# Kernel optimization log

Measured on AMD Instinct MI355X. Metric: run time of the kernel, lower is better.

## Reference

```python
import jax, jax.numpy as jnp
from jax import lax
import numpy as np

B, V, H, K, E = 256, 30000, 512, 200, 300
SH_ALPHA = 20.0
REC_W = 0.7
N_ITERS = 100       # fixed iteration budget (original caps at 5000; convergence check freezes updates)
STOP_THR = 0.005
BN_EPS = 1e-3


def setup_inputs() -> dict:
    key = jax.random.key(0)
    ks = jax.random.split(key, 8)
    n = lambda k, shape, scale: (jax.random.normal(k, shape, jnp.float32) * scale)
    return {
        "bows": jax.random.uniform(ks[0], (B, V), jnp.float32),
        "W1": n(ks[1], (H, V), 0.01),
        "b1": jnp.zeros((H,), jnp.float32),
        "W2": n(ks[2], (K, H), 0.05),
        "b2": jnp.zeros((K,), jnp.float32),
        "gamma": jnp.ones((K,), jnp.float32),
        "beta": jnp.zeros((K,), jnp.float32),
        "word_emb": n(ks[3], (V, E), 0.1),
        "topic_emb": n(ks[4], (K, E), 0.1),
    }


def _l2norm(x):
    return x / jnp.maximum(jnp.linalg.norm(x, axis=1, keepdims=True), 1e-12)


def _sinkhorn(cost, kernel, a, b):
    # a: [K,B], b: [V,B], kernel: [K,V]
    u0 = jnp.ones_like(a) / a.shape[0]
    v0 = jnp.ones_like(b)

    def body(carry, i):
        u, v, err = carry
        active = err > STOP_THR
        # u = a / (kernel @ (b / (u^T kernel)^T))
        u1 = a / (kernel @ (b / (u.T @ kernel).T))

        def check(_):
            v1 = b / (kernel.T @ u1)
            u2 = a / (kernel @ v1)
            bb = v1 * (kernel.T @ u2)
            e = jnp.max(jnp.sum(jnp.abs(bb - b), axis=0))
            return u2, v1, e

        # original does the v-refresh + err check when steps % 20 == 1 (steps = i+1)
        u1, v1, e1 = lax.cond(i % 20 == 0, check, lambda _: (u1, v, err), None)
        u = jnp.where(active, u1, u)
        v = jnp.where(active, v1, v)
        err = jnp.where(active, e1, err)
        return (u, v, err), None

    (u, v, _), _ = lax.scan(jax.checkpoint(body), (u0, v0, jnp.asarray(1.0, a.dtype)),
                            jnp.arange(N_ITERS))
    # per-document sinkhorn cost: sum_k u * ((kernel*cost) @ v)
    return jnp.sum(u * ((kernel * cost) @ v), axis=0)  # [B]


def reference(bows, W1, b1, W2, b2, gamma, beta, word_emb, topic_emb):
    # encoder (training-mode BN with batch stats; dropout disabled for determinism)
    h = jax.nn.relu(bows @ W1.T + b1)                      # [B,H]
    z = h @ W2.T + b2                                      # [B,K]
    mu = jnp.mean(z, axis=0)
    var = jnp.var(z, axis=0)                               # biased, as torch BN uses
    zn = gamma * (z - mu) / jnp.sqrt(var + BN_EPS) + beta
    doc_topic = jax.nn.softmax(zn, axis=1)                 # [B,K]

    topic_word = _l2norm(topic_emb) @ _l2norm(word_emb).T  # [K,V]
    cost = 1.0 - topic_word
    kernel = jnp.exp(-cost * SH_ALPHA)

    doc_word = jax.nn.softmax(bows, axis=1)                # [B,V]
    sinkhorn_loss = _sinkhorn(cost, kernel, doc_topic.T, doc_word.T).mean()

    rec_log_probs = jax.nn.log_softmax(doc_topic @ topic_word, axis=1)  # [B,V]
    reconstruction_loss = -(rec_log_probs * bows).sum(axis=1).mean()
    return REC_W * reconstruction_loss, sinkhorn_loss
```

## Files before the change

kernel.cpp:

```cpp
#include <hip/hip_runtime.h>
#include <math.h>

#define CDIV(a,b) (((a)+(b)-1)/(b))

typedef unsigned short u16;
typedef unsigned long long u64;
typedef __attribute__((ext_vector_type(8))) short bf16x8;
typedef __attribute__((ext_vector_type(4))) float f32x4;

constexpr int Bn = 256;
constexpr int Vn = 30000;
constexpr int Hn = 512;
constexpr int Kn = 200;
constexpr int En = 300;
constexpr int E3 = 320;
constexpr int Kp = 224;
constexpr int Vc = 224;
constexpr int NCH = 136;
constexpr int CPX = NCH / 8;
constexpr int Vpad = NCH * Vc;
constexpr int SW1 = 32;
constexpr float ALPHA  = 20.0f;
constexpr float RECW   = 0.7f;
constexpr float THRC   = 0.005f;
constexpr float EPS_BN = 1e-3f;
constexpr int   NIT    = 100;

__device__ __forceinline__ float bf2f(u16 h) {
  union { unsigned u; float f; } c; c.u = (unsigned)h << 16; return c.f;
}
__device__ __forceinline__ u16 f2bf(float f) {
  union { float f; unsigned u; } c; c.f = f;
  return (u16)((c.u + 0x7fffu + ((c.u >> 16) & 1u)) >> 16);
}
__device__ __forceinline__ bf16x8 load8bf(const float* p) {
  float4 a = *(const float4*)p, b = *(const float4*)(p + 4);
  bf16x8 r;
  r[0] = (short)f2bf(a.x); r[1] = (short)f2bf(a.y);
  r[2] = (short)f2bf(a.z); r[3] = (short)f2bf(a.w);
  r[4] = (short)f2bf(b.x); r[5] = (short)f2bf(b.y);
  r[6] = (short)f2bf(b.z); r[7] = (short)f2bf(b.w);
  return r;
}

template<int MODE>
__global__ __launch_bounds__(256, 3)
void fusedAB(const u16* __restrict__ kernT, const u16* __restrict__ kernA,
             const u16* __restrict__ ub, const u16* __restrict__ bmb,
             u16* __restrict__ wout, const u16* __restrict__ win,
             u16* __restrict__ tpart, float* __restrict__ errp,
             const int* __restrict__ frozen)
{
  if (MODE != 3 && frozen[0]) return;
  const int bid = blockIdx.x;
  const int xcd = bid & 7, wid = bid >> 3;
  const int c = xcd * CPX + (wid >> 2), g = wid & 3;
  const int v0 = c * Vc, b0 = g * 64;
  const int tid = threadIdx.x;
  const int wv = tid >> 6, l = tid & 63, l15 = l & 15, lg = l >> 4;
  const int rloc = wv * 16 + l15;
  const int bcol = b0 + rloc;
  __shared__ u16 wlds[64 * Vc];
  char* wbase = (char*)wlds;
  const int sw = (rloc & 3) << 4;

  if (MODE != 3) {
    bf16x8 uf[7];
    {
      const u16* up = ub + (size_t)bcol * Kp + lg * 8;
#pragma unroll
      for (int ks = 0; ks < 7; ++ks) uf[ks] = *(const bf16x8*)(up + ks * 32);
    }
    float e = 0.f;
    for (int vt = 0; vt < Vc / 16; ++vt) {
      const u16* ktp = kernT + (size_t)(v0 + vt * 16 + l15) * Kp + lg * 8;
      f32x4 acc = {0.f, 0.f, 0.f, 0.f};
#pragma unroll
      for (int ks = 0; ks < 7; ++ks) {
        bf16x8 kf = *(const bf16x8*)(ktp + ks * 32);
        acc = __builtin_amdgcn_mfma_f32_16x16x32_bf16(kf, uf[ks], acc, 0, 0, 0);
      }
      const int vbase = v0 + vt * 16 + lg * 4;
      const size_t po = (size_t)bcol * Vpad + vbase;
      u64 bq = *(const u64*)(bmb + po);
      if (MODE == 2) {
        u64 wq = *(const u64*)(win + po);
#pragma unroll
        for (int r = 0; r < 4; ++r) {
          float bm = bf2f((u16)(bq >> (16 * r)));
          float wv_ = bf2f((u16)(wq >> (16 * r)));
          e += fabsf(wv_ * acc[r] - bm);
        }
      } else {
        u64 wq = 0;
#pragma unroll
        for (int r = 0; r < 4; ++r) {
          float bm = bf2f((u16)(bq >> (16 * r)));
          float w = (vbase + r < Vn) ? bm / acc[r] : 0.f;
          wq |= (u64)f2bf(w) << (16 * r);
        }
        *(u64*)(wbase + rloc * (Vc * 2) + ((vt * 32 + lg * 8) ^ sw)) = wq;
        if (MODE == 1) *(u64*)(wout + po) = wq;
      }
    }
    if (MODE == 2) {
      e += __shfl_xor(e, 16, 64);
      e += __shfl_xor(e, 32, 64);
      if (l < 16) errp[c * Bn + bcol] = e;
      return;
    }
    __syncthreads();
  }

  f32x4 accB[13];
#pragma unroll
  for (int mt = 0; mt < 13; ++mt) accB[mt] = (f32x4){0.f, 0.f, 0.f, 0.f};
  for (int vs = 0; vs < Vc / 32; ++vs) {
    bf16x8 wf;
    if (MODE == 3) wf = *(const bf16x8*)(win + (size_t)bcol * Vpad + v0 + vs * 32 + lg * 8);
    else wf = *(const bf16x8*)(wbase + rloc * (Vc * 2) + (((vs * 32 + lg * 8) * 2) ^ sw));
    const u16* kap = kernA + (size_t)l15 * Vpad + v0 + vs * 32 + lg * 8;
#pragma unroll
    for (int mt = 0; mt < 13; ++mt) {
      bf16x8 af = *(const bf16x8*)(kap + (size_t)mt * 16 * Vpad);
      accB[mt] = __builtin_amdgcn_mfma_f32_16x16x32_bf16(af, wf, accB[mt], 0, 0, 0);
    }
  }
#pragma unroll
  for (int mt = 0; mt < 13; ++mt) {
#pragma unroll
    for (int r = 0; r < 4; ++r) {
      int k = mt * 16 + lg * 4 + r;
      if (k < Kn) tpart[((size_t)c * Kn + k) * Bn + bcol] = f2bf(accB[mt][r]);
    }
  }
}

__global__ __launch_bounds__(256, 2)
void reconMF(const u16* __restrict__ costT, const u16* __restrict__ dtb,
             u16* __restrict__ rbuf)
{
  const int c = blockIdx.x, g = blockIdx.y;
  const int v0 = c * Vc, b0 = g * 64;
  const int tid = threadIdx.x;
  const int wv = tid >> 6, l = tid & 63, l15 = l & 15, lg = l >> 4;
  const int bcol = b0 + wv * 16 + l15;
  bf16x8 uf[7];
  {
    const u16* up = dtb + (size_t)bcol * Kp + lg * 8;
#pragma unroll
    for (int ks = 0; ks < 7; ++ks) uf[ks] = *(const bf16x8*)(up + ks * 32);
  }
  for (int vt = 0; vt < Vc / 16; ++vt) {
    const u16* ktp = costT + (size_t)(v0 + vt * 16 + l15) * Kp + lg * 8;
    f32x4 acc = {0.f, 0.f, 0.f, 0.f};
#pragma unroll
    for (int ks = 0; ks < 7; ++ks) {
      bf16x8 kf = *(const bf16x8*)(ktp + ks * 32);
      acc = __builtin_amdgcn_mfma_f32_16x16x32_bf16(kf, uf[ks], acc, 0, 0, 0);
    }
    const int vbase = v0 + vt * 16 + lg * 4;
    u64 q = 0;
#pragma unroll
    for (int r = 0; r < 4; ++r) q |= (u64)f2bf(1.f - acc[r]) << (16 * r);
    *(u64*)(rbuf + (size_t)bcol * Vpad + vbase) = q;
  }
}

__global__ __launch_bounds__(256)
void gemmTW(const u16* __restrict__ nth, const u16* __restrict__ ntl,
            const u16* __restrict__ nwh, const u16* __restrict__ nwl,
            u16* __restrict__ kern_bf, u16* __restrict__ kc_bf,
            u16* __restrict__ cost_bf)
{
  const int n0 = blockIdx.x * 64;
  const int tid = threadIdx.x;
  const int wv = tid >> 6, l = tid & 63, l15 = l & 15, lg = l >> 4;
  const int n = n0 + wv * 16 + l15;
  const bool nok = n < Vn;
  f32x4 acc[14];
#pragma unroll
  for (int mt = 0; mt < 14; ++mt) acc[mt] = (f32x4){0.f, 0.f, 0.f, 0.f};
  for (int kc = 0; kc < E3; kc += 32) {
    bf16x8 bh = {0,0,0,0,0,0,0,0}, bl = {0,0,0,0,0,0,0,0};
    if (nok) {
      const size_t o = (size_t)n * E3 + kc + lg * 8;
      bh = *(const bf16x8*)(nwh + o);
      bl = *(const bf16x8*)(nwl + o);
    }
#pragma unroll
    for (int mt = 0; mt < 14; ++mt) {
      const size_t ao = (size_t)(mt * 16 + l15) * E3 + kc + lg * 8;
      bf16x8 ah = *(const bf16x8*)(nth + ao);
      bf16x8 al = *(const bf16x8*)(ntl + ao);
      acc[mt] = __builtin_amdgcn_mfma_f32_16x16x32_bf16(ah, bh, acc[mt], 0, 0, 0);
      acc[mt] = __builtin_amdgcn_mfma_f32_16x16x32_bf16(ah, bl, acc[mt], 0, 0, 0);
      acc[mt] = __builtin_amdgcn_mfma_f32_16x16x32_bf16(al, bh, acc[mt], 0, 0, 0);
    }
  }
#pragma unroll
  for (int mt = 0; mt < 14; ++mt) {
#pragma unroll
    for (int r = 0; r < 4; ++r) {
      int k = mt * 16 + lg * 4 + r;
      float cf = 1.f - acc[mt][r];
      float kf = expf(-ALPHA * cf);
      size_t o = (size_t)k * Vpad + n;
      kern_bf[o] = f2bf(kf);
      kc_bf[o]   = f2bf(kf * cf);
      cost_bf[o] = f2bf(cf);
    }
  }
}

__global__ __launch_bounds__(256)
void gemmW1(const float* __restrict__ A, const float* __restrict__ B,
            float* __restrict__ part)
{
  const int bid = blockIdx.x;
  const int xcd = bid & 7, wid = bid >> 3;
  const int s = xcd * 4 + (wid >> 3);
  const int nx = wid & 7;
  const int n0 = nx * 64, k0 = s * 960;
  const int tid = threadIdx.x;
  const int wv = tid >> 6, l = tid & 63, l15 = l & 15, lg = l >> 4;
  f32x4 acc[4][4];
#pragma unroll
  for (int i = 0; i < 4; ++i)
#pragma unroll
    for (int j = 0; j < 4; ++j) acc[i][j] = (f32x4){0.f, 0.f, 0.f, 0.f};
  for (int kc = k0; kc < k0 + 960; kc += 32) {
    const int kk = kc + lg * 8;
    const bool ok = kk < Vn;
    bf16x8 af[4], bf[4];
#pragma unroll
    for (int mt = 0; mt < 4; ++mt) {
      const int m = wv * 64 + mt * 16 + l15;
      af[mt] = ok ? load8bf(A + (size_t)m * Vn + kk) : (bf16x8){0,0,0,0,0,0,0,0};
    }
#pragma unroll
    for (int nt = 0; nt < 4; ++nt) {
      const int n = n0 + nt * 16 + l15;
      bf[nt] = ok ? load8bf(B + (size_t)n * Vn + kk) : (bf16x8){0,0,0,0,0,0,0,0};
    }
#pragma unroll
    for (int mt = 0; mt < 4; ++mt)
#pragma unroll
      for (int nt = 0; nt < 4; ++nt)
        acc[mt][nt] = __builtin_amdgcn_mfma_f32_16x16x32_bf16(af[mt], bf[nt], acc[mt][nt], 0, 0, 0);
  }
#pragma unroll
  for (int mt = 0; mt < 4; ++mt)
#pragma unroll
    for (int nt = 0; nt < 4; ++nt)
#pragma unroll
      for (int r = 0; r < 4; ++r) {
        const int m = wv * 64 + mt * 16 + lg * 4 + r;
        const int n = n0 + nt * 16 + l15;
        part[(size_t)s * (Bn * Hn) + (size_t)m * Hn + n] = acc[mt][nt][r];
      }
}

__global__ void transposeK(const u16* __restrict__ src, u16* __restrict__ dst)
{
  __shared__ u16 t[32][33];
  int tx = threadIdx.x & 31, ty = threadIdx.x >> 5;
  int v0 = blockIdx.x * 32, k0 = blockIdx.y * 32;
#pragma unroll
  for (int r = 0; r < 4; ++r) t[ty + 8 * r][tx] = src[(size_t)(k0 + ty + 8 * r) * Vpad + v0 + tx];
  __syncthreads();
#pragma unroll
  for (int r = 0; r < 4; ++r) dst[(size_t)(v0 + ty + 8 * r) * Kp + k0 + tx] = t[tx][ty + 8 * r];
}

__global__ void convTemb(const float* __restrict__ temb, const float* __restrict__ rnT,
                         u16* __restrict__ nth, u16* __restrict__ ntl)
{
  int k = blockIdx.x, e = threadIdx.x;
  float v = (k < Kn && e < En) ? temb[(size_t)k * En + e] * rnT[k] : 0.f;
  u16 hi = f2bf(v);
  nth[(size_t)k * E3 + e] = hi;
  ntl[(size_t)k * E3 + e] = f2bf(v - bf2f(hi));
}

__global__ void convWemb(const float* __restrict__ wemb, const float* __restrict__ rnW,
                         u16* __restrict__ nwh, u16* __restrict__ nwl)
{
  for (size_t idx = (size_t)blockIdx.x * 256 + threadIdx.x; idx < (size_t)Vn * E3;
       idx += (size_t)gridDim.x * 256) {
    int v = (int)(idx / E3), e = (int)(idx - (size_t)v * E3);
    float x = (e < En) ? wemb[(size_t)v * En + e] * rnW[v] : 0.f;
    u16 hi = f2bf(x);
    nwh[idx] = hi;
    nwl[idx] = f2bf(x - bf2f(hi));
  }
}

__global__ __launch_bounds__(256)
void gemm_nt(const float* __restrict__ A, const float* __restrict__ Bm,
             float* __restrict__ P, int M, int N, int Kd)
{
  const int S = gridDim.z, s = blockIdx.z;
  const int k0 = (int)((long long)Kd * s / S);
  const int k1 = (int)((long long)Kd * (s + 1) / S);
  const int m0 = blockIdx.y * 64, n0 = blockIdx.x * 64;
  __shared__ float As[16][68];
  __shared__ float Bs[16][68];
  const int tid = threadIdx.x;
  const int tx = tid & 15, ty = tid >> 4;
  const int lrow = tid >> 2, lkg = (tid & 3) * 4;
  const int mi = m0 + lrow, ni = n0 + lrow;
  float acc[4][4] = {};
  for (int kc = k0; kc < k1; kc += 16) {
    float4 a4 = {0.f, 0.f, 0.f, 0.f}, b4 = {0.f, 0.f, 0.f, 0.f};
    if (mi < M) a4 = *(const float4*)&A[(size_t)mi * Kd + kc + lkg];
    if (ni < N) b4 = *(const float4*)&Bm[(size_t)ni * Kd + kc + lkg];
    As[lkg + 0][lrow] = a4.x; As[lkg + 1][lrow] = a4.y;
    As[lkg + 2][lrow] = a4.z; As[lkg + 3][lrow] = a4.w;
    Bs[lkg + 0][lrow] = b4.x; Bs[lkg + 1][lrow] = b4.y;
    Bs[lkg + 2][lrow] = b4.z; Bs[lkg + 3][lrow] = b4.w;
    __syncthreads();
#pragma unroll
    for (int kk = 0; kk < 16; ++kk) {
      float4 av = *(const float4*)&As[kk][ty * 4];
      float4 bv = *(const float4*)&Bs[kk][tx * 4];
      float a_[4] = {av.x, av.y, av.z, av.w};
      float b_[4] = {bv.x, bv.y, bv.z, bv.w};
#pragma unroll
      for (int i = 0; i < 4; ++i)
#pragma unroll
        for (int j = 0; j < 4; ++j)
          acc[i][j] += a_[i] * b_[j];
    }
    __syncthreads();
  }
  const size_t base = (size_t)s * M * N;
#pragma unroll
  for (int i = 0; i < 4; ++i) {
    int m = m0 + ty * 4 + i;
    if (m >= M) continue;
#pragma unroll
    for (int j = 0; j < 4; ++j) {
      int n = n0 + tx * 4 + j;
      if (n < N) P[base + (size_t)m * N + n] = acc[i][j];
    }
  }
}

__global__ void rowNorms(const float* __restrict__ X, float* __restrict__ rn, int R, int C)
{
  int wv = threadIdx.x >> 6, lane = threadIdx.x & 63;
  int r = blockIdx.x * 4 + wv;
  if (r >= R) return;
  float s = 0.f;
  for (int c = lane; c < C; c += 64) { float x = X[(size_t)r * C + c]; s += x * x; }
#pragma unroll
  for (int m = 32; m; m >>= 1) s += __shfl_xor(s, m, 64);
  if (lane == 0) rn[r] = 1.f / fmaxf(sqrtf(s), 1e-12f);
}

__global__ void epiH(const float* __restrict__ P, const float* __restrict__ b1,
                     float* __restrict__ h, int S)
{
  int i = blockIdx.x * blockDim.x + threadIdx.x;
  if (i >= Bn * Hn) return;
  float v = b1[i & (Hn - 1)];
  for (int s = 0; s < S; ++s) v += P[(size_t)s * Bn * Hn + i];
  h[i] = fmaxf(v, 0.f);
}

__global__ void bnStats(const float* __restrict__ P, const float* __restrict__ b2,
                        float* __restrict__ mu, float* __restrict__ ivar, int S)
{
  int k = blockIdx.x, b = threadIdx.x;
  float z = b2[k];
  for (int s = 0; s < S; ++s) z += P[((size_t)s * Bn + b) * Kn + k];
  __shared__ float r1[256], r2[256];
  r1[b] = z; r2[b] = z * z; __syncthreads();
  for (int st = 128; st; st >>= 1) {
    if (b < st) { r1[b] += r1[b + st]; r2[b] += r2[b + st]; }
    __syncthreads();
  }
  if (b == 0) {
    float m = r1[0] / Bn, v = r2[0] / Bn - (r1[0] / Bn) * (r1[0] / Bn);
    mu[k] = m; ivar[k] = rsqrtf(v + EPS_BN);
  }
}

__global__ void bnSoftmax(const float* __restrict__ P, const float* __restrict__ b2,
                          const float* __restrict__ mu, const float* __restrict__ ivar,
                          const float* __restrict__ gamma, const float* __restrict__ beta,
                          float* __restrict__ a, u16* __restrict__ dtb, int S)
{
  int b = blockIdx.x, k = threadIdx.x;
  float zn = -1e30f;
  if (k < Kn) {
    float z = b2[k];
    for (int s = 0; s < S; ++s) z += P[((size_t)s * Bn + b) * Kn + k];
    zn = gamma[k] * (z - mu[k]) * ivar[k] + beta[k];
  }
  __shared__ float red[256];
  red[k] = zn; __syncthreads();
  for (int st = 128; st; st >>= 1) { if (k < st) red[k] = fmaxf(red[k], red[k + st]); __syncthreads(); }
  float mx = red[0]; __syncthreads();
  float e = (k < Kn) ? expf(zn - mx) : 0.f;
  red[k] = e; __syncthreads();
  for (int st = 128; st; st >>= 1) { if (k < st) red[k] += red[k + st]; __syncthreads(); }
  float dt = e / red[0];
  if (k < Kn) a[(size_t)k * Bn + b] = dt;
  if (k < Kp) dtb[(size_t)b * Kp + k] = (k < Kn) ? f2bf(dt) : (u16)0;
}

__global__ __launch_bounds__(512)
void rowSoftmax2(const float* __restrict__ bows, u16* __restrict__ bmb)
{
  int b = blockIdx.x, t = threadIdx.x;
  const float4* row = (const float4*)(bows + (size_t)b * Vn);
  __shared__ float red[512];
  float mx = -1e30f;
  for (int v4 = t; v4 < Vn / 4; v4 += 512) {
    float4 x = row[v4];
    mx = fmaxf(mx, fmaxf(fmaxf(x.x, x.y), fmaxf(x.z, x.w)));
  }
  red[t] = mx; __syncthreads();
  for (int st = 256; st; st >>= 1) { if (t < st) red[t] = fmaxf(red[t], red[t + st]); __syncthreads(); }
  mx = red[0]; __syncthreads();
  float sum = 0.f;
  for (int v4 = t; v4 < Vn / 4; v4 += 512) {
    float4 x = row[v4];
    sum += expf(x.x - mx) + expf(x.y - mx) + expf(x.z - mx) + expf(x.w - mx);
  }
  red[t] = sum; __syncthreads();
  for (int st = 256; st; st >>= 1) { if (t < st) red[t] += red[t + st]; __syncthreads(); }
  float inv = 1.f / red[0];
  for (int v4 = t; v4 < Vn / 4; v4 += 512) {
    float4 x = row[v4];
    u64 q = (u64)f2bf(expf(x.x - mx) * inv)
          | ((u64)f2bf(expf(x.y - mx) * inv) << 16)
          | ((u64)f2bf(expf(x.z - mx) * inv) << 32)
          | ((u64)f2bf(expf(x.w - mx) * inv) << 48);
    *(u64*)(bmb + (size_t)b * Vpad + v4 * 4) = q;
  }
  for (int p = t; p < (Vpad - Vn) / 4; p += 512)
    *(u64*)(bmb + (size_t)b * Vpad + Vn + p * 4) = 0;
}

__global__ void initU2(u16* __restrict__ ub)
{
  int b = blockIdx.x, k = threadIdx.x;
  ub[(size_t)b * Kp + k] = (k < Kn) ? f2bf(1.f / Kn) : (u16)0;
}

__global__ void updateU2(const u16* __restrict__ tpart, const float* __restrict__ a,
                         u16* __restrict__ ub, const int* __restrict__ frozen)
{
  if (frozen[0]) return;
  int i = blockIdx.x * 256 + threadIdx.x;
  int k = i >> 6, b0 = (i & 63) * 4;
  float t0 = 0.f, t1 = 0.f, t2_ = 0.f, t3 = 0.f;
  for (int c = 0; c < NCH; ++c) {
    u64 q = *(const u64*)(tpart + ((size_t)c * Kn + k) * Bn + b0);
    t0 += bf2f((u16)q);        t1 += bf2f((u16)(q >> 16));
    t2_ += bf2f((u16)(q >> 32)); t3 += bf2f((u16)(q >> 48));
  }
  float4 av = *(const float4*)&a[(size_t)k * Bn + b0];
  ub[(size_t)(b0 + 0) * Kp + k] = f2bf(av.x / t0);
  ub[(size_t)(b0 + 1) * Kp + k] = f2bf(av.y / t1);
  ub[(size_t)(b0 + 2) * Kp + k] = f2bf(av.z / t2_);
  ub[(size_t)(b0 + 3) * Kp + k] = f2bf(av.w / t3);
}

__global__ void sumT(const u16* __restrict__ tpart, float* __restrict__ t2)
{
  int i = blockIdx.x * 256 + threadIdx.x;
  int k = i >> 6, b0 = (i & 63) * 4;
  float4 t = {0.f, 0.f, 0.f, 0.f};
  for (int c = 0; c < NCH; ++c) {
    u64 q = *(const u64*)(tpart + ((size_t)c * Kn + k) * Bn + b0);
    t.x += bf2f((u16)q);         t.y += bf2f((u16)(q >> 16));
    t.z += bf2f((u16)(q >> 32)); t.w += bf2f((u16)(q >> 48));
  }
  *(float4*)&t2[(size_t)k * Bn + b0] = t;
}

__global__ void errFin(const float* __restrict__ errp, int nc, int* __restrict__ frozen)
{
  if (frozen[0]) return;
  int b = threadIdx.x;
  float s = 0.f;
  for (int c = 0; c < nc; ++c) s += errp[(size_t)c * Bn + b];
  __shared__ float red[256];
  red[b] = s; __syncthreads();
  for (int st = 128; st; st >>= 1) { if (b < st) red[b] = fmaxf(red[b], red[b + st]); __syncthreads(); }
  if (b == 0 && red[0] <= THRC) frozen[0] = 1;
}

__global__ __launch_bounds__(512)
void recPass2(const u16* __restrict__ r, const float* __restrict__ bows,
              float* __restrict__ Lb)
{
  int b = blockIdx.x, t = threadIdx.x;
  const float m = 1.0f;
  const float4* br = (const float4*)(bows + (size_t)b * Vn);
  float se = 0.f, dot = 0.f, bs = 0.f;
  for (int v4 = t; v4 < Vn / 4; v4 += 512) {
    u64 q = *(const u64*)(r + (size_t)b * Vpad + v4 * 4);
    float4 w = br[v4];
    float x0 = bf2f((u16)q), x1 = bf2f((u16)(q >> 16));
    float x2 = bf2f((u16)(q >> 32)), x3 = bf2f((u16)(q >> 48));
    se  += expf(x0 - m) + expf(x1 - m) + expf(x2 - m) + expf(x3 - m);
    dot += w.x * x0 + w.y * x1 + w.z * x2 + w.w * x3;
    bs  += w.x + w.y + w.z + w.w;
  }
  __shared__ float red[512];
  red[t] = se; __syncthreads();
  for (int st = 256; st; st >>= 1) { if (t < st) red[t] += red[t + st]; __syncthreads(); }
  float seT = red[0]; __syncthreads();
  red[t] = dot; __syncthreads();
  for (int st = 256; st; st >>= 1) { if (t < st) red[t] += red[t + st]; __syncthreads(); }
  float dotT = red[0]; __syncthreads();
  red[t] = bs; __syncthreads();
  for (int st = 256; st; st >>= 1) { if (t < st) red[t] += red[t + st]; __syncthreads(); }
  if (t == 0) Lb[b] = dotT - (m + logf(seT)) * red[0];
}

__global__ void finalOut(const u16* __restrict__ ub, const float* __restrict__ t2,
                         const float* __restrict__ Lb, float* __restrict__ outp)
{
  int b = threadIdx.x;
  float sl = 0.f;
  for (int k = 0; k < Kn; ++k) sl += bf2f(ub[(size_t)b * Kp + k]) * t2[(size_t)k * Bn + b];
  __shared__ float r1[256], r2[256];
  r1[b] = sl; r2[b] = Lb[b]; __syncthreads();
  for (int st = 128; st; st >>= 1) {
    if (b < st) { r1[b] += r1[b + st]; r2[b] += r2[b + st]; }
    __syncthreads();
  }
  if (b == 0) {
    outp[0] = RECW * (-(r2[0] / (float)Bn));
    outp[1] = r1[0] / (float)Bn;
  }
}

extern "C" void kernel_launch(void* const* d_in, const int* in_sizes, int n_in,
                              void* d_out, int out_size, void* d_ws, size_t ws_size,
                              hipStream_t stream)
{
  const float* bows  = (const float*)d_in[0];
  const float* W1    = (const float*)d_in[1];
  const float* b1    = (const float*)d_in[2];
  const float* W2    = (const float*)d_in[3];
  const float* b2    = (const float*)d_in[4];
  const float* gamma = (const float*)d_in[5];
  const float* beta  = (const float*)d_in[6];
  const float* wemb  = (const float*)d_in[7];
  const float* temb  = (const float*)d_in[8];
  float* out = (float*)d_out;

  float* ws = (float*)d_ws;
  size_t off = 0;
  auto alloc = [&](size_t n) { float* p = ws + off; off += (n + 63) & ~(size_t)63; return p; };
  float* wbuf    = alloc((size_t)SW1 * Bn * Hn);
  u16*   kern_bf = (u16*)alloc(((size_t)Kp * Vpad + 1) / 2);
  u16*   kernT   = (u16*)alloc(((size_t)Vpad * Kp + 1) / 2);
  u16*   kc_bf   = (u16*)alloc(((size_t)Kp * Vpad + 1) / 2);
  u16*   cost_bf = (u16*)alloc(((size_t)Kp * Vpad + 1) / 2);
  u16*   costT   = (u16*)alloc(((size_t)Vpad * Kp + 1) / 2);
  u16*   nw_hi   = (u16*)alloc(((size_t)Vn * E3 + 1) / 2);
  u16*   nw_lo   = (u16*)alloc(((size_t)Vn * E3 + 1) / 2);
  u16*   nt_hi   = (u16*)alloc(((size_t)Kp * E3 + 1) / 2);
  u16*   nt_lo   = (u16*)alloc(((size_t)Kp * E3 + 1) / 2);
  u16*   ub_bf   = (u16*)alloc(((size_t)Bn * Kp + 1) / 2);
  u16*   dt_bf   = (u16*)alloc(((size_t)Bn * Kp + 1) / 2);
  u16*   tpart   = (u16*)alloc(((size_t)NCH * Kn * Bn + 1) / 2);
  float* hbuf    = alloc((size_t)Bn * Hn);
  float* abuf    = alloc((size_t)Kn * Bn);
  float* t2      = alloc((size_t)Kn * Bn);
  float* rnT     = alloc(Kn);
  float* rnW     = alloc(Vn);
  float* mu      = alloc(Kn);
  float* ivar    = alloc(Kn);
  float* errp    = alloc((size_t)NCH * Bn);
  float* Lb      = alloc(Bn);
  int* frozen = (int*)(ws + off); off += 64;
  if (off * sizeof(float) > ws_size) return;
  u16* bm_bf = nw_hi;
  u16* vb_bf = nw_lo;
  u16* rbuf  = kern_bf;

  hipMemsetAsync(frozen, 0, sizeof(int), stream);

  rowNorms<<<CDIV(Kn, 4), 256, 0, stream>>>(temb, rnT, Kn, En);
  rowNorms<<<CDIV(Vn, 4), 256, 0, stream>>>(wemb, rnW, Vn, En);
  convTemb<<<Kp, E3, 0, stream>>>(temb, rnT, nt_hi, nt_lo);
  convWemb<<<4096, 256, 0, stream>>>(wemb, rnW, nw_hi, nw_lo);
  gemmTW<<<Vpad / 64, 256, 0, stream>>>(nt_hi, nt_lo, nw_hi, nw_lo, kern_bf, kc_bf, cost_bf);
  transposeK<<<dim3(Vpad / 32, Kp / 32), 256, 0, stream>>>(kern_bf, kernT);
  transposeK<<<dim3(Vpad / 32, Kp / 32), 256, 0, stream>>>(cost_bf, costT);

  gemmW1<<<8 * SW1, 256, 0, stream>>>(bows, W1, wbuf);
  epiH<<<CDIV(Bn * Hn, 256), 256, 0, stream>>>(wbuf, b1, hbuf, SW1);
  {
    dim3 g(CDIV(Kn, 64), CDIV(Bn, 64), 4);
    gemm_nt<<<g, 256, 0, stream>>>(hbuf, W2, wbuf, Bn, Kn, Hn);
  }
  bnStats<<<Kn, 256, 0, stream>>>(wbuf, b2, mu, ivar, 4);
  bnSoftmax<<<Bn, 256, 0, stream>>>(wbuf, b2, mu, ivar, gamma, beta, abuf, dt_bf, 4);
  rowSoftmax2<<<Bn, 512, 0, stream>>>(bows, bm_bf);
  initU2<<<Bn, Kp, 0, stream>>>(ub_bf);

  const int gF = NCH * 4;
  const int gU = (Kn * 64) / 256;
  for (int it = 0; it < NIT; ++it) {
    fusedAB<0><<<gF, 256, 0, stream>>>(kernT, kern_bf, ub_bf, bm_bf, nullptr, nullptr, tpart, nullptr, frozen);
    updateU2<<<gU, 256, 0, stream>>>(tpart, abuf, ub_bf, frozen);
    if (it % 20 == 0) {
      fusedAB<1><<<gF, 256, 0, stream>>>(kernT, kern_bf, ub_bf, bm_bf, vb_bf, nullptr, tpart, nullptr, frozen);
      updateU2<<<gU, 256, 0, stream>>>(tpart, abuf, ub_bf, frozen);
      fusedAB<2><<<gF, 256, 0, stream>>>(kernT, kern_bf, ub_bf, bm_bf, nullptr, vb_bf, tpart, errp, frozen);
      errFin<<<1, 256, 0, stream>>>(errp, NCH, frozen);
    }
  }

  reconMF<<<dim3(NCH, Bn / 64), 256, 0, stream>>>(costT, dt_bf, rbuf);
  recPass2<<<Bn, 512, 0, stream>>>(rbuf, bows, Lb);

  fusedAB<3><<<gF, 256, 0, stream>>>(nullptr, kc_bf, ub_bf, nullptr, nullptr, vb_bf, tpart, nullptr, frozen);
  sumT<<<gU, 256, 0, stream>>>(tpart, t2);
  finalOut<<<1, 256, 0, stream>>>(ub_bf, t2, Lb, out);
}
```

Before: 2.484 ms.

## Parallelize sinkhorn reductions, double-buffer W1 GEMM, split K finer, retune occupancy

updateU2 and sumT now run one block per topic row, with four waves each summing a quarter of the chunk partials and combining them through LDS. The old layout used only 50 blocks and serial 136-step loops, and this change targets the latency of that per-iteration reduction. gemmW1 doubles its split-K count and halves the slice length, and it now prefetches the next K step into a second register set while the MFMAs run. fusedAB's launch bounds drop from 3 to 2 waves per SIMD, and workspace buffers are aliased into one shared region. The larger split-K doubles the partial-sum traffic that epiH has to reduce.

```diff
diff --git a/kernel.cpp b/kernel.cpp
--- a/kernel.cpp
+++ b/kernel.cpp
@@ -19,7 +19,8 @@
 constexpr int NCH = 136;
 constexpr int CPX = NCH / 8;
 constexpr int Vpad = NCH * Vc;
-constexpr int SW1 = 32;
+constexpr int SW1 = 64;
+constexpr int KSL = 480;
 constexpr float ALPHA  = 20.0f;
 constexpr float RECW   = 0.7f;
 constexpr float THRC   = 0.005f;
@@ -44,7 +45,7 @@
 }
 
 template<int MODE>
-__global__ __launch_bounds__(256, 3)
+__global__ __launch_bounds__(256, 2)
 void fusedAB(const u16* __restrict__ kernT, const u16* __restrict__ kernA,
              const u16* __restrict__ ub, const u16* __restrict__ bmb,
              u16* __restrict__ wout, const u16* __restrict__ win,
@@ -218,10 +219,10 @@
             float* __restrict__ part)
 {
   const int bid = blockIdx.x;
-  const int xcd = bid & 7, wid = bid >> 3;
-  const int s = xcd * 4 + (wid >> 3);
-  const int nx = wid & 7;
-  const int n0 = nx * 64, k0 = s * 960;
+  const int xcd = bid & 7, t = bid >> 3;
+  const int s = xcd * 8 + (t >> 3);
+  const int nx = t & 7;
+  const int n0 = nx * 64, k0 = s * KSL;
   const int tid = threadIdx.x;
   const int wv = tid >> 6, l = tid & 63, l15 = l & 15, lg = l >> 4;
   f32x4 acc[4][4];
@@ -229,26 +230,44 @@
   for (int i = 0; i < 4; ++i)
 #pragma unroll
     for (int j = 0; j < 4; ++j) acc[i][j] = (f32x4){0.f, 0.f, 0.f, 0.f};
-  for (int kc = k0; kc < k0 + 960; kc += 32) {
-    const int kk = kc + lg * 8;
-    const bool ok = kk < Vn;
-    bf16x8 af[4], bf[4];
-#pragma unroll
-    for (int mt = 0; mt < 4; ++mt) {
-      const int m = wv * 64 + mt * 16 + l15;
-      af[mt] = ok ? load8bf(A + (size_t)m * Vn + kk) : (bf16x8){0,0,0,0,0,0,0,0};
-    }
-#pragma unroll
-    for (int nt = 0; nt < 4; ++nt) {
-      const int n = n0 + nt * 16 + l15;
-      bf[nt] = ok ? load8bf(B + (size_t)n * Vn + kk) : (bf16x8){0,0,0,0,0,0,0,0};
-    }
-#pragma unroll
-    for (int mt = 0; mt < 4; ++mt)
-#pragma unroll
-      for (int nt = 0; nt < 4; ++nt)
-        acc[mt][nt] = __builtin_amdgcn_mfma_f32_16x16x32_bf16(af[mt], bf[nt], acc[mt][nt], 0, 0, 0);
-  }
+
+  bf16x8 aA[4], bA[4], aB[4], bB[4];
+
+#define LDW1(KC, AF, BF)                                                        \
+  { const int kk_ = (KC) + lg * 8;                                              \
+    const bool ok_ = kk_ < Vn;                                                  \
+    _Pragma("unroll")                                                           \
+    for (int mt = 0; mt < 4; ++mt) {                                            \
+      const int m_ = wv * 64 + mt * 16 + l15;                                   \
+      AF[mt] = ok_ ? load8bf(A + (size_t)m_ * Vn + kk_) : (bf16x8){0,0,0,0,0,0,0,0}; \
+    }                                                                           \
+    _Pragma("unroll")                                                           \
+    for (int nt = 0; nt < 4; ++nt) {                                            \
+      const int n_ = n0 + nt * 16 + l15;                                        \
+      BF[nt] = ok_ ? load8bf(B + (size_t)n_ * Vn + kk_) : (bf16x8){0,0,0,0,0,0,0,0}; \
+    } }
+
+#define FMAW1(AF, BF)                                                           \
+  _Pragma("unroll")                                                             \
+  for (int mt = 0; mt < 4; ++mt)                                                \
+    _Pragma("unroll")                                                           \
+    for (int nt = 0; nt < 4; ++nt)                                              \
+      acc[mt][nt] = __builtin_amdgcn_mfma_f32_16x16x32_bf16(AF[mt], BF[nt], acc[mt][nt], 0, 0, 0);
+
+  LDW1(k0, aA, bA);
+#pragma unroll
+  for (int step = 0; step < KSL / 32; ++step) {
+    if ((step & 1) == 0) {
+      if (step + 1 < KSL / 32) LDW1(k0 + (step + 1) * 32, aB, bB);
+      FMAW1(aA, bA);
+    } else {
+      if (step + 1 < KSL / 32) LDW1(k0 + (step + 1) * 32, aA, bA);
+      FMAW1(aB, bB);
+    }
+  }
+#undef LDW1
+#undef FMAW1
+
 #pragma unroll
   for (int mt = 0; mt < 4; ++mt)
 #pragma unroll
@@ -365,6 +384,7 @@
   int i = blockIdx.x * blockDim.x + threadIdx.x;
   if (i >= Bn * Hn) return;
   float v = b1[i & (Hn - 1)];
+#pragma unroll 8
   for (int s = 0; s < S; ++s) v += P[(size_t)s * Bn * Hn + i];
   h[i] = fmaxf(v, 0.f);
 }
@@ -451,36 +471,63 @@
   ub[(size_t)b * Kp + k] = (k < Kn) ? f2bf(1.f / Kn) : (u16)0;
 }
 
-__global__ void updateU2(const u16* __restrict__ tpart, const float* __restrict__ a,
-                         u16* __restrict__ ub, const int* __restrict__ frozen)
+__global__ __launch_bounds__(256)
+void updateU2(const u16* __restrict__ tpart, const float* __restrict__ a,
+              u16* __restrict__ ub, const int* __restrict__ frozen)
 {
   if (frozen[0]) return;
-  int i = blockIdx.x * 256 + threadIdx.x;
-  int k = i >> 6, b0 = (i & 63) * 4;
-  float t0 = 0.f, t1 = 0.f, t2_ = 0.f, t3 = 0.f;
-  for (int c = 0; c < NCH; ++c) {
-    u64 q = *(const u64*)(tpart + ((size_t)c * Kn + k) * Bn + b0);
-    t0 += bf2f((u16)q);        t1 += bf2f((u16)(q >> 16));
-    t2_ += bf2f((u16)(q >> 32)); t3 += bf2f((u16)(q >> 48));
-  }
-  float4 av = *(const float4*)&a[(size_t)k * Bn + b0];
-  ub[(size_t)(b0 + 0) * Kp + k] = f2bf(av.x / t0);
-  ub[(size_t)(b0 + 1) * Kp + k] = f2bf(av.y / t1);
-  ub[(size_t)(b0 + 2) * Kp + k] = f2bf(av.z / t2_);
-  ub[(size_t)(b0 + 3) * Kp + k] = f2bf(av.w / t3);
-}
-
-__global__ void sumT(const u16* __restrict__ tpart, float* __restrict__ t2)
-{
-  int i = blockIdx.x * 256 + threadIdx.x;
-  int k = i >> 6, b0 = (i & 63) * 4;
-  float4 t = {0.f, 0.f, 0.f, 0.f};
-  for (int c = 0; c < NCH; ++c) {
-    u64 q = *(const u64*)(tpart + ((size_t)c * Kn + k) * Bn + b0);
-    t.x += bf2f((u16)q);         t.y += bf2f((u16)(q >> 16));
-    t.z += bf2f((u16)(q >> 32)); t.w += bf2f((u16)(q >> 48));
-  }
-  *(float4*)&t2[(size_t)k * Bn + b0] = t;
+  const int k = blockIdx.x;
+  const int cg = threadIdx.x >> 6, q = threadIdx.x & 63;
+  const int b0 = q * 4;
+  f32x4 t = {0.f, 0.f, 0.f, 0.f};
+  for (int c = cg * (NCH / 4); c < (cg + 1) * (NCH / 4); ++c) {
+    u64 qd = *(const u64*)(tpart + ((size_t)c * Kn + k) * Bn + b0);
+    t[0] += bf2f((u16)qd);         t[1] += bf2f((u16)(qd >> 16));
+    t[2] += bf2f((u16)(qd >> 32)); t[3] += bf2f((u16)(qd >> 48));
+  }
+  __shared__ f32x4 red[4][64];
+  red[cg][q] = t;
+  __syncthreads();
+  if (cg == 0) {
+    f32x4 s = red[0][q];
+#pragma unroll
+    for (int gg = 1; gg < 4; ++gg) {
+      f32x4 o = red[gg][q];
+      s[0] += o[0]; s[1] += o[1]; s[2] += o[2]; s[3] += o[3];
+    }
+    float4 av = *(const float4*)&a[(size_t)k * Bn + b0];
+    ub[(size_t)(b0 + 0) * Kp + k] = f2bf(av.x / s[0]);
+    ub[(size_t)(b0 + 1) * Kp + k] = f2bf(av.y / s[1]);
+    ub[(size_t)(b0 + 2) * Kp + k] = f2bf(av.z / s[2]);
+    ub[(size_t)(b0 + 3) * Kp + k] = f2bf(av.w / s[3]);
+  }
+}
+
+__global__ __launch_bounds__(256)
+void sumT(const u16* __restrict__ tpart, float* __restrict__ t2)
+{
+  const int k = blockIdx.x;
+  const int cg = threadIdx.x >> 6, q = threadIdx.x & 63;
+  const int b0 = q * 4;
+  f32x4 t = {0.f, 0.f, 0.f, 0.f};
+  for (int c = cg * (NCH / 4); c < (cg + 1) * (NCH / 4); ++c) {
+    u64 qd = *(const u64*)(tpart + ((size_t)c * Kn + k) * Bn + b0);
+    t[0] += bf2f((u16)qd);         t[1] += bf2f((u16)(qd >> 16));
+    t[2] += bf2f((u16)(qd >> 32)); t[3] += bf2f((u16)(qd >> 48));
+  }
+  __shared__ f32x4 red[4][64];
+  red[cg][q] = t;
+  __syncthreads();
+  if (cg == 0) {
+    f32x4 s = red[0][q];
+#pragma unroll
+    for (int gg = 1; gg < 4; ++gg) {
+      f32x4 o = red[gg][q];
+      s[0] += o[0]; s[1] += o[1]; s[2] += o[2]; s[3] += o[3];
+    }
+    float4 ov; ov.x = s[0]; ov.y = s[1]; ov.z = s[2]; ov.w = s[3];
+    *(float4*)&t2[(size_t)k * Bn + b0] = ov;
+  }
 }
 
 __global__ void errFin(const float* __restrict__ errp, int nc, int* __restrict__ frozen)
@@ -560,19 +607,20 @@
   float* ws = (float*)d_ws;
   size_t off = 0;
   auto alloc = [&](size_t n) { float* p = ws + off; off += (n + 63) & ~(size_t)63; return p; };
-  float* wbuf    = alloc((size_t)SW1 * Bn * Hn);
+  size_t r1_floats = (size_t)Vn * E3;
+  if ((size_t)SW1 * Bn * Hn > r1_floats) r1_floats = (size_t)SW1 * Bn * Hn;
+  float* R1      = alloc(r1_floats);
   u16*   kern_bf = (u16*)alloc(((size_t)Kp * Vpad + 1) / 2);
   u16*   kernT   = (u16*)alloc(((size_t)Vpad * Kp + 1) / 2);
   u16*   kc_bf   = (u16*)alloc(((size_t)Kp * Vpad + 1) / 2);
   u16*   cost_bf = (u16*)alloc(((size_t)Kp * Vpad + 1) / 2);
   u16*   costT   = (u16*)alloc(((size_t)Vpad * Kp + 1) / 2);
-  u16*   nw_hi   = (u16*)alloc(((size_t)Vn * E3 + 1) / 2);
-  u16*   nw_lo   = (u16*)alloc(((size_t)Vn * E3 + 1) / 2);
   u16*   nt_hi   = (u16*)alloc(((size_t)Kp * E3 + 1) / 2);
   u16*   nt_lo   = (u16*)alloc(((size_t)Kp * E3 + 1) / 2);
   u16*   ub_bf   = (u16*)alloc(((size_t)Bn * Kp + 1) / 2);
   u16*   dt_bf   = (u16*)alloc(((size_t)Bn * Kp + 1) / 2);
   u16*   tpart   = (u16*)alloc(((size_t)NCH * Kn * Bn + 1) / 2);
+  float* w2buf   = alloc((size_t)4 * Bn * Kn);
   float* hbuf    = alloc((size_t)Bn * Hn);
   float* abuf    = alloc((size_t)Kn * Bn);
   float* t2      = alloc((size_t)Kn * Bn);
@@ -584,9 +632,12 @@
   float* Lb      = alloc(Bn);
   int* frozen = (int*)(ws + off); off += 64;
   if (off * sizeof(float) > ws_size) return;
-  u16* bm_bf = nw_hi;
-  u16* vb_bf = nw_lo;
-  u16* rbuf  = kern_bf;
+  u16*   nw_hi  = (u16*)R1;
+  u16*   nw_lo  = nw_hi + (size_t)Vn * E3;
+  float* w1part = R1;
+  u16*   bm_bf  = (u16*)R1;
+  u16*   vb_bf  = bm_bf + (size_t)Bn * Vpad;
+  u16*   rbuf   = kern_bf;
 
   hipMemsetAsync(frozen, 0, sizeof(int), stream);
 
@@ -598,25 +649,24 @@
   transposeK<<<dim3(Vpad / 32, Kp / 32), 256, 0, stream>>>(kern_bf, kernT);
   transposeK<<<dim3(Vpad / 32, Kp / 32), 256, 0, stream>>>(cost_bf, costT);
 
-  gemmW1<<<8 * SW1, 256, 0, stream>>>(bows, W1, wbuf);
-  epiH<<<CDIV(Bn * Hn, 256), 256, 0, stream>>>(wbuf, b1, hbuf, SW1);
+  gemmW1<<<8 * SW1, 256, 0, stream>>>(bows, W1, w1part);
+  epiH<<<CDIV(Bn * Hn, 256), 256, 0, stream>>>(w1part, b1, hbuf, SW1);
   {
     dim3 g(CDIV(Kn, 64), CDIV(Bn, 64), 4);
-    gemm_nt<<<g, 256, 0, stream>>>(hbuf, W2, wbuf, Bn, Kn, Hn);
-  }
-  bnStats<<<Kn, 256, 0, stream>>>(wbuf, b2, mu, ivar, 4);
-  bnSoftmax<<<Bn, 256, 0, stream>>>(wbuf, b2, mu, ivar, gamma, beta, abuf, dt_bf, 4);
+    gemm_nt<<<g, 256, 0, stream>>>(hbuf, W2, w2buf, Bn, Kn, Hn);
+  }
+  bnStats<<<Kn, 256, 0, stream>>>(w2buf, b2, mu, ivar, 4);
+  bnSoftmax<<<Bn, 256, 0, stream>>>(w2buf, b2, mu, ivar, gamma, beta, abuf, dt_bf, 4);
   rowSoftmax2<<<Bn, 512, 0, stream>>>(bows, bm_bf);
   initU2<<<Bn, Kp, 0, stream>>>(ub_bf);
 
   const int gF = NCH * 4;
-  const int gU = (Kn * 64) / 256;
   for (int it = 0; it < NIT; ++it) {
     fusedAB<0><<<gF, 256, 0, stream>>>(kernT, kern_bf, ub_bf, bm_bf, nullptr, nullptr, tpart, nullptr, frozen);
-    updateU2<<<gU, 256, 0, stream>>>(tpart, abuf, ub_bf, frozen);
+    updateU2<<<Kn, 256, 0, stream>>>(tpart, abuf, ub_bf, frozen);
     if (it % 20 == 0) {
       fusedAB<1><<<gF, 256, 0, stream>>>(kernT, kern_bf, ub_bf, bm_bf, vb_bf, nullptr, tpart, nullptr, frozen);
-      updateU2<<<gU, 256, 0, stream>>>(tpart, abuf, ub_bf, frozen);
+      updateU2<<<Kn, 256, 0, stream>>>(tpart, abuf, ub_bf, frozen);
       fusedAB<2><<<gF, 256, 0, stream>>>(kernT, kern_bf, ub_bf, bm_bf, nullptr, vb_bf, tpart, errp, frozen);
       errFin<<<1, 256, 0, stream>>>(errp, NCH, frozen);
     }
@@ -626,6 +676,6 @@
   recPass2<<<Bn, 512, 0, stream>>>(rbuf, bows, Lb);
 
   fusedAB<3><<<gF, 256, 0, stream>>>(nullptr, kc_bf, ub_bf, nullptr, nullptr, vb_bf, tpart, nullptr, frozen);
-  sumT<<<gU, 256, 0, stream>>>(tpart, t2);
+  sumT<<<Kn, 256, 0, stream>>>(tpart, t2);
   finalOut<<<1, 256, 0, stream>>>(ub_bf, t2, Lb, out);
 }
```

Measured after the change: 2.312 ms. -6.9%, faster.
